# Kernel optimization log

Measured on AMD Instinct MI355X. Metric: run time of the kernel, lower is better.

Reference implementation:

```python
import jax, jax.numpy as jnp
import numpy as np

HEADS = 8
DIM_HEAD = 32
SCALE = DIM_HEAD ** -0.5


def setup_inputs() -> dict:
    key = jax.random.key(0)
    ks = jax.random.split(key, 5)
    b, c, H, W = 4, 256, 48, 48
    n = H * W
    hidden = HEADS * DIM_HEAD
    x = jax.random.normal(ks[0], (b, c, H, W), dtype=jnp.float32)
    pos_bias = jax.random.normal(ks[1], (HEADS, n, n), dtype=jnp.float32) * 0.02
    w_qkv = jax.random.normal(ks[2], (hidden * 3, c), dtype=jnp.float32) * (c ** -0.5)
    w_out = jax.random.normal(ks[3], (c, hidden), dtype=jnp.float32) * (hidden ** -0.5)
    b_out = jax.random.normal(ks[4], (c,), dtype=jnp.float32) * 0.01
    return {"x": x, "pos_bias": pos_bias, "w_qkv": w_qkv, "w_out": w_out, "b_out": b_out}


def reference(x, pos_bias, w_qkv, w_out, b_out):
    b, c, H, W = x.shape
    n = H * W
    xf = x.reshape(b, c, n)                                  # [b, c, n]
    qkv = jnp.einsum('oc,bcn->bon', w_qkv, xf)               # 1x1 conv, no bias
    q, k, v = jnp.split(qkv, 3, axis=1)                      # each [b, hidden, n]
    def to_heads(t):
        return t.reshape(b, HEADS, DIM_HEAD, n)              # b h d n
    q, k, v = to_heads(q) * SCALE, to_heads(k), to_heads(v)
    sim = jnp.einsum('bhdi,bhdj->bhij', q, k)                # [b, h, n, n]
    sim = sim + pos_bias[None]                               # broadcast over batch
    attn = jax.nn.softmax(sim, axis=-1)
    out = jnp.einsum('bhij,bhdj->bhid', attn, v)             # [b, h, n, d]
    out = out.transpose(0, 1, 3, 2).reshape(b, HEADS * DIM_HEAD, n)  # b (h d) n
    out = jnp.einsum('oc,bcn->bon', w_out, out) + b_out[None, :, None]
    return out.reshape(b, c, H, W)
```

## Files before the change

### kernel.cpp

```cpp
#include <hip/hip_runtime.h>
#include <stdint.h>
#include <stddef.h>

#define BB 4
#define CC 256
#define NH 8
#define DH 32
#define NN 2304
#define O3 768
#define HID 256
#define QK_SCALE 0.17677669529663687f
#define LOG2E 1.44269504f

typedef __attribute__((ext_vector_type(8))) short short8;
typedef __attribute__((ext_vector_type(4))) float float4v;

__device__ __forceinline__ unsigned short f2bf(float f) {
    union { float f; uint32_t u; } v; v.f = f;
    uint32_t u = v.u;
    return (unsigned short)((u + 0x7FFFu + ((u >> 16) & 1u)) >> 16);
}
__device__ __forceinline__ float bf2f(unsigned short s) {
    union { uint32_t u; float f; } v; v.u = ((uint32_t)s) << 16;
    return v.f;
}

__global__ void cast_weights(const float* __restrict__ wqkv,
                             const float* __restrict__ wout,
                             unsigned short* __restrict__ whi,
                             unsigned short* __restrict__ wlo,
                             unsigned short* __restrict__ wob) {
    int i = blockIdx.x * 256 + threadIdx.x;
    float wv = wqkv[i];
    unsigned short hi = f2bf(wv);
    whi[i] = hi;
    wlo[i] = f2bf(wv - bf2f(hi));
    if (i < HID * HID) wob[i] = f2bf(wout[i]);
}

__global__ __launch_bounds__(256) void transpose_x(const float* __restrict__ x,
                                                   unsigned short* __restrict__ xT) {
    const int n0 = blockIdx.x * 32, c0 = blockIdx.y * 32, b = blockIdx.z;
    __shared__ float ls[32][33];
    const int t = threadIdx.x;
    {
        int c = t >> 3, nc = (t & 7) * 4;
        float4 v4 = *(const float4*)(x + ((size_t)b * CC + c0 + c) * NN + n0 + nc);
        ls[c][nc] = v4.x; ls[c][nc + 1] = v4.y; ls[c][nc + 2] = v4.z; ls[c][nc + 3] = v4.w;
    }
    __syncthreads();
    {
        int n = t >> 3, cl = (t & 7) * 4;
        uint32_t p0 = (uint32_t)f2bf(ls[cl + 0][n]) | ((uint32_t)f2bf(ls[cl + 1][n]) << 16);
        uint32_t p1 = (uint32_t)f2bf(ls[cl + 2][n]) | ((uint32_t)f2bf(ls[cl + 3][n]) << 16);
        uint32_t* dst = (uint32_t*)(xT + ((size_t)b * NN + n0 + n) * CC + c0 + cl);
        dst[0] = p0; dst[1] = p1;
    }
}

__global__ __launch_bounds__(256) void qkv_gemm_bf16(const unsigned short* __restrict__ xT,
                                                     const unsigned short* __restrict__ whi,
                                                     const unsigned short* __restrict__ wlo,
                                                     unsigned short* __restrict__ q,
                                                     unsigned short* __restrict__ k,
                                                     unsigned short* __restrict__ v) {
    const int og = blockIdx.x;
    const int n0 = blockIdx.y * 64;
    const int b  = blockIdx.z;
    const int t = threadIdx.x;
    const int w = t >> 6, lane = t & 63, l15 = lane & 15, quad = lane >> 4;
    const unsigned short* xb = xT + (size_t)b * NN * CC;

    float4v acc[4] = {{0.f,0.f,0.f,0.f},{0.f,0.f,0.f,0.f},
                      {0.f,0.f,0.f,0.f},{0.f,0.f,0.f,0.f}};

    if (og < 8) {
        const int o0 = og * 64;
        const unsigned short* ap = xb + (size_t)(n0 + w * 16 + l15) * CC + quad * 8;
        #pragma unroll
        for (int c0 = 0; c0 < CC; c0 += 32) {
            short8 af = *(const short8*)(ap + c0);
            #pragma unroll
            for (int jj = 0; jj < 4; ++jj) {
                const size_t wo = (size_t)(o0 + jj * 16 + l15) * CC + c0 + quad * 8;
                short8 bh = *(const short8*)(whi + wo);
                short8 bl = *(const short8*)(wlo + wo);
                acc[jj] = __builtin_amdgcn_mfma_f32_16x16x32_bf16(af, bh, acc[jj], 0, 0, 0);
                acc[jj] = __builtin_amdgcn_mfma_f32_16x16x32_bf16(af, bl, acc[jj], 0, 0, 0);
            }
        }
        #pragma unroll
        for (int jj = 0; jj < 4; ++jj) {
            const int o = o0 + jj * 16 + l15;
            const int which = o >> 8;
            const int h = (o >> 5) & 7, d = o & 31;
            unsigned short* dst = which ? k : q;
            const float sc = which ? 1.0f : QK_SCALE * LOG2E;
            #pragma unroll
            for (int r = 0; r < 4; ++r) {
                const int n = n0 + w * 16 + quad * 4 + r;
                dst[(((size_t)b * NH + h) * NN + n) * DH + d] = f2bf(acc[jj][r] * sc);
            }
        }
    } else {
        const int o0 = 512 + (og - 8) * 64;
        const size_t wr = (size_t)(o0 + w * 16 + l15) * CC + quad * 8;
        #pragma unroll
        for (int c0 = 0; c0 < CC; c0 += 32) {
            short8 ah = *(const short8*)(whi + wr + c0);
            short8 al = *(const short8*)(wlo + wr + c0);
            #pragma unroll
            for (int jj = 0; jj < 4; ++jj) {
                short8 bf = *(const short8*)(xb + (size_t)(n0 + jj * 16 + l15) * CC + c0 + quad * 8);
                acc[jj] = __builtin_amdgcn_mfma_f32_16x16x32_bf16(ah, bf, acc[jj], 0, 0, 0);
                acc[jj] = __builtin_amdgcn_mfma_f32_16x16x32_bf16(al, bf, acc[jj], 0, 0, 0);
            }
        }
        #pragma unroll
        for (int r = 0; r < 4; ++r) {
            const int o = o0 + w * 16 + quad * 4 + r;
            const int h = (o >> 5) & 7, d = o & 31;
            #pragma unroll
            for (int jj = 0; jj < 4; ++jj) {
                const int n = n0 + jj * 16 + l15;
                v[(((size_t)b * NH + h) * DH + d) * NN + n] = f2bf(acc[jj][r]);
            }
        }
    }
}

__global__ __launch_bounds__(256) void attn_kernel(const unsigned short* __restrict__ qg,
                                                   const unsigned short* __restrict__ kg,
                                                   const unsigned short* __restrict__ vg,
                                                   const float* __restrict__ bias,
                                                   unsigned short* __restrict__ ao) {
    const int i0   = blockIdx.x * 16;
    const int h    = blockIdx.y;
    const int t    = threadIdx.x;
    const int w    = t >> 6;
    const int lane = t & 63;
    const int l15  = lane & 15;
    const int quad = lane >> 4;

    __shared__ unsigned short ps[4][16][136];

    const size_t bh = (size_t)w * NH + h;
    const unsigned short* qp = qg + bh * NN * DH;
    const unsigned short* kp = kg + bh * NN * DH;
    const unsigned short* vp = vg + bh * DH * NN;

    short8 qf = *(const short8*)(qp + (size_t)(i0 + l15) * DH + quad * 8);

    float4v oa0 = {0.f, 0.f, 0.f, 0.f};
    float4v oa1 = {0.f, 0.f, 0.f, 0.f};
    float4v zero = {0.f, 0.f, 0.f, 0.f};
    float l_r[4] = {0.f, 0.f, 0.f, 0.f};

    const float* bp = bias + ((size_t)h * NN + i0 + quad * 4) * NN + l15;

    float bcur[4][8];
    #pragma unroll
    for (int r = 0; r < 4; ++r)
        #pragma unroll
        for (int jj = 0; jj < 8; ++jj)
            bcur[r][jj] = bp[(size_t)r * NN + jj * 16] * LOG2E;

    for (int jt = 0; jt < NN; jt += 128) {
        float bnext[4][8];
        if (jt + 128 < NN) {
            #pragma unroll
            for (int r = 0; r < 4; ++r)
                #pragma unroll
                for (int jj = 0; jj < 8; ++jj)
                    bnext[r][jj] = bp[(size_t)r * NN + jt + 128 + jj * 16] * LOG2E;
        }

        float4v s[8];
        #pragma unroll
        for (int jj = 0; jj < 8; ++jj) {
            short8 kf = *(const short8*)(kp + (size_t)(jt + jj * 16 + l15) * DH + quad * 8);
            s[jj] = __builtin_amdgcn_mfma_f32_16x16x32_bf16(qf, kf, zero, 0, 0, 0);
        }

        #pragma unroll
        for (int r = 0; r < 4; ++r) {
            const int row = quad * 4 + r;
            #pragma unroll
            for (int jj = 0; jj < 8; ++jj) {
                float p = exp2f(s[jj][r] + bcur[r][jj]);
                l_r[r] += p;
                ps[w][row][jj * 16 + l15] = f2bf(p);
            }
        }

        #pragma unroll
        for (int c = 0; c < 4; ++c) {
            short8 pa = *(const short8*)&ps[w][l15][c * 32 + quad * 8];
            short8 v0 = *(const short8*)(vp + (size_t)l15 * NN        + jt + c * 32 + quad * 8);
            short8 v1 = *(const short8*)(vp + (size_t)(l15 + 16) * NN + jt + c * 32 + quad * 8);
            oa0 = __builtin_amdgcn_mfma_f32_16x16x32_bf16(pa, v0, oa0, 0, 0, 0);
            oa1 = __builtin_amdgcn_mfma_f32_16x16x32_bf16(pa, v1, oa1, 0, 0, 0);
        }

        if (jt + 128 < NN) {
            #pragma unroll
            for (int r = 0; r < 4; ++r)
                #pragma unroll
                for (int jj = 0; jj < 8; ++jj)
                    bcur[r][jj] = bnext[r][jj];
        }
    }

    #pragma unroll
    for (int r = 0; r < 4; ++r) {
        #pragma unroll
        for (int off = 1; off < 16; off <<= 1)
            l_r[r] += __shfl_xor(l_r[r], off, 64);
    }

    unsigned short* aop = ao + ((size_t)w * NN + i0) * HID + h * DH;
    #pragma unroll
    for (int r = 0; r < 4; ++r) {
        const int row = quad * 4 + r;
        const float inv = 1.0f / l_r[r];
        aop[(size_t)row * HID + l15]      = f2bf(oa0[r] * inv);
        aop[(size_t)row * HID + 16 + l15] = f2bf(oa1[r] * inv);
    }
}

__global__ __launch_bounds__(256) void out_proj(const unsigned short* __restrict__ wob,
                                                const unsigned short* __restrict__ aob,
                                                const float* __restrict__ bout,
                                                float* __restrict__ out) {
    const int n0 = blockIdx.x * 64;
    const int o0 = blockIdx.y * 64;
    const int b  = blockIdx.z;
    const int t = threadIdx.x;
    const int w = t >> 6, lane = t & 63, l15 = lane & 15, quad = lane >> 4;
    const int orow = o0 + w * 16;

    float4v acc[4] = {{0.f,0.f,0.f,0.f},{0.f,0.f,0.f,0.f},
                      {0.f,0.f,0.f,0.f},{0.f,0.f,0.f,0.f}};
    const unsigned short* ap = aob + ((size_t)b * NN + n0) * HID;
    #pragma unroll
    for (int c0 = 0; c0 < HID; c0 += 32) {
        short8 af = *(const short8*)(wob + (size_t)(orow + l15) * HID + c0 + quad * 8);
        #pragma unroll
        for (int jj = 0; jj < 4; ++jj) {
            short8 bf = *(const short8*)(ap + (size_t)(jj * 16 + l15) * HID + c0 + quad * 8);
            acc[jj] = __builtin_amdgcn_mfma_f32_16x16x32_bf16(af, bf, acc[jj], 0, 0, 0);
        }
    }
    float* op = out + (size_t)b * HID * NN;
    #pragma unroll
    for (int r = 0; r < 4; ++r) {
        const int o = orow + quad * 4 + r;
        const float bv = bout[o];
        #pragma unroll
        for (int jj = 0; jj < 4; ++jj)
            op[(size_t)o * NN + n0 + jj * 16 + l15] = acc[jj][r] + bv;
    }
}

extern "C" void kernel_launch(void* const* d_in, const int* in_sizes, int n_in,
                              void* d_out, int out_size, void* d_ws, size_t ws_size,
                              hipStream_t stream) {
    const float* x        = (const float*)d_in[0];
    const float* pos_bias = (const float*)d_in[1];
    const float* w_qkv    = (const float*)d_in[2];
    const float* w_out    = (const float*)d_in[3];
    const float* b_out    = (const float*)d_in[4];
    float* out = (float*)d_out;

    char* ws = (char*)d_ws;
    unsigned short* xT  = (unsigned short*)(ws);
    unsigned short* q   = (unsigned short*)(ws + 4718592);
    unsigned short* k   = (unsigned short*)(ws + 9437184);
    unsigned short* v   = (unsigned short*)(ws + 14155776);
    unsigned short* ao  = (unsigned short*)(ws + 18874368);
    unsigned short* wob = (unsigned short*)(ws + 23592960);
    unsigned short* whi = (unsigned short*)(ws + 23724032);
    unsigned short* wlo = (unsigned short*)(ws + 24117248);

    cast_weights<<<O3 * CC / 256, 256, 0, stream>>>(w_qkv, w_out, whi, wlo, wob);
    transpose_x<<<dim3(NN / 32, CC / 32, BB), 256, 0, stream>>>(x, xT);
    qkv_gemm_bf16<<<dim3(12, NN / 64, BB), 256, 0, stream>>>(xT, whi, wlo, q, k, v);
    attn_kernel<<<dim3(NN / 16, NH), 256, 0, stream>>>(q, k, v, pos_bias, ao);
    out_proj<<<dim3(NN / 64, HID / 64, BB), 256, 0, stream>>>(wob, ao, b_out, out);
}
```

Measured before the change: 506.5 us.

## Split attention blocks per batch, drop bias prefetch, fuse prep kernels

The attention kernel previously used 256-thread blocks where each wave handled one batch and all four waves shared the same positional-bias rows through cache. It now launches one 64-thread block per (query tile, head, batch), drops the software double-buffered bias prefetch in favour of loading bias at each tile, and merges the weight cast and x transpose into one prep kernel. This lowers register pressure and adds more independent blocks, but loses the intra-block sharing of bias loads across batches and the explicit load/compute overlap, so bias traffic may rise.

```diff
diff --git a/kernel.cpp b/kernel.cpp
--- a/kernel.cpp
+++ b/kernel.cpp
@@ -25,36 +25,38 @@
     return v.f;
 }
 
-__global__ void cast_weights(const float* __restrict__ wqkv,
-                             const float* __restrict__ wout,
-                             unsigned short* __restrict__ whi,
-                             unsigned short* __restrict__ wlo,
-                             unsigned short* __restrict__ wob) {
-    int i = blockIdx.x * 256 + threadIdx.x;
-    float wv = wqkv[i];
-    unsigned short hi = f2bf(wv);
-    whi[i] = hi;
-    wlo[i] = f2bf(wv - bf2f(hi));
-    if (i < HID * HID) wob[i] = f2bf(wout[i]);
-}
-
-__global__ __launch_bounds__(256) void transpose_x(const float* __restrict__ x,
-                                                   unsigned short* __restrict__ xT) {
-    const int n0 = blockIdx.x * 32, c0 = blockIdx.y * 32, b = blockIdx.z;
-    __shared__ float ls[32][33];
+__global__ __launch_bounds__(256) void prep_kernel(const float* __restrict__ x,
+                                                   const float* __restrict__ wqkv,
+                                                   const float* __restrict__ wout,
+                                                   unsigned short* __restrict__ xT,
+                                                   unsigned short* __restrict__ whi,
+                                                   unsigned short* __restrict__ wlo,
+                                                   unsigned short* __restrict__ wob) {
+    const int bid = blockIdx.x;
     const int t = threadIdx.x;
-    {
-        int c = t >> 3, nc = (t & 7) * 4;
-        float4 v4 = *(const float4*)(x + ((size_t)b * CC + c0 + c) * NN + n0 + nc);
-        ls[c][nc] = v4.x; ls[c][nc + 1] = v4.y; ls[c][nc + 2] = v4.z; ls[c][nc + 3] = v4.w;
-    }
-    __syncthreads();
-    {
-        int n = t >> 3, cl = (t & 7) * 4;
-        uint32_t p0 = (uint32_t)f2bf(ls[cl + 0][n]) | ((uint32_t)f2bf(ls[cl + 1][n]) << 16);
-        uint32_t p1 = (uint32_t)f2bf(ls[cl + 2][n]) | ((uint32_t)f2bf(ls[cl + 3][n]) << 16);
-        uint32_t* dst = (uint32_t*)(xT + ((size_t)b * NN + n0 + n) * CC + c0 + cl);
-        dst[0] = p0; dst[1] = p1;
+    if (bid < 2304) {
+        const int n0 = (bid % 72) * 32, c0 = ((bid / 72) % 8) * 32, b = bid / 576;
+        __shared__ float ls[32][33];
+        {
+            int c = t >> 3, nc = (t & 7) * 4;
+            float4 v4 = *(const float4*)(x + ((size_t)b * CC + c0 + c) * NN + n0 + nc);
+            ls[c][nc] = v4.x; ls[c][nc + 1] = v4.y; ls[c][nc + 2] = v4.z; ls[c][nc + 3] = v4.w;
+        }
+        __syncthreads();
+        {
+            int n = t >> 3, cl = (t & 7) * 4;
+            uint32_t p0 = (uint32_t)f2bf(ls[cl + 0][n]) | ((uint32_t)f2bf(ls[cl + 1][n]) << 16);
+            uint32_t p1 = (uint32_t)f2bf(ls[cl + 2][n]) | ((uint32_t)f2bf(ls[cl + 3][n]) << 16);
+            uint32_t* dst = (uint32_t*)(xT + ((size_t)b * NN + n0 + n) * CC + c0 + cl);
+            dst[0] = p0; dst[1] = p1;
+        }
+    } else {
+        int i = (bid - 2304) * 256 + t;
+        float wv = wqkv[i];
+        unsigned short hi = f2bf(wv);
+        whi[i] = hi;
+        wlo[i] = f2bf(wv - bf2f(hi));
+        if (i < HID * HID) wob[i] = f2bf(wout[i]);
     }
 }
 
@@ -129,22 +131,21 @@
     }
 }
 
-__global__ __launch_bounds__(256) void attn_kernel(const unsigned short* __restrict__ qg,
-                                                   const unsigned short* __restrict__ kg,
-                                                   const unsigned short* __restrict__ vg,
-                                                   const float* __restrict__ bias,
-                                                   unsigned short* __restrict__ ao) {
+__global__ __launch_bounds__(64) void attn_kernel(const unsigned short* __restrict__ qg,
+                                                  const unsigned short* __restrict__ kg,
+                                                  const unsigned short* __restrict__ vg,
+                                                  const float* __restrict__ bias,
+                                                  unsigned short* __restrict__ ao) {
     const int i0   = blockIdx.x * 16;
     const int h    = blockIdx.y;
-    const int t    = threadIdx.x;
-    const int w    = t >> 6;
-    const int lane = t & 63;
+    const int b    = blockIdx.z;
+    const int lane = threadIdx.x;
     const int l15  = lane & 15;
     const int quad = lane >> 4;
 
-    __shared__ unsigned short ps[4][16][136];
-
-    const size_t bh = (size_t)w * NH + h;
+    __shared__ unsigned short ps[16][136];
+
+    const size_t bh = (size_t)b * NH + h;
     const unsigned short* qp = qg + bh * NN * DH;
     const unsigned short* kp = kg + bh * NN * DH;
     const unsigned short* vp = vg + bh * DH * NN;
@@ -158,22 +159,13 @@
 
     const float* bp = bias + ((size_t)h * NN + i0 + quad * 4) * NN + l15;
 
-    float bcur[4][8];
-    #pragma unroll
-    for (int r = 0; r < 4; ++r)
-        #pragma unroll
-        for (int jj = 0; jj < 8; ++jj)
-            bcur[r][jj] = bp[(size_t)r * NN + jj * 16] * LOG2E;
-
     for (int jt = 0; jt < NN; jt += 128) {
-        float bnext[4][8];
-        if (jt + 128 < NN) {
-            #pragma unroll
-            for (int r = 0; r < 4; ++r)
-                #pragma unroll
-                for (int jj = 0; jj < 8; ++jj)
-                    bnext[r][jj] = bp[(size_t)r * NN + jt + 128 + jj * 16] * LOG2E;
-        }
+        float bcur[4][8];
+        #pragma unroll
+        for (int r = 0; r < 4; ++r)
+            #pragma unroll
+            for (int jj = 0; jj < 8; ++jj)
+                bcur[r][jj] = bp[(size_t)r * NN + jt + jj * 16] * LOG2E;
 
         float4v s[8];
         #pragma unroll
@@ -189,26 +181,18 @@
             for (int jj = 0; jj < 8; ++jj) {
                 float p = exp2f(s[jj][r] + bcur[r][jj]);
                 l_r[r] += p;
-                ps[w][row][jj * 16 + l15] = f2bf(p);
+                ps[row][jj * 16 + l15] = f2bf(p);
             }
         }
 
         #pragma unroll
         for (int c = 0; c < 4; ++c) {
-            short8 pa = *(const short8*)&ps[w][l15][c * 32 + quad * 8];
+            short8 pa = *(const short8*)&ps[l15][c * 32 + quad * 8];
             short8 v0 = *(const short8*)(vp + (size_t)l15 * NN        + jt + c * 32 + quad * 8);
             short8 v1 = *(const short8*)(vp + (size_t)(l15 + 16) * NN + jt + c * 32 + quad * 8);
             oa0 = __builtin_amdgcn_mfma_f32_16x16x32_bf16(pa, v0, oa0, 0, 0, 0);
             oa1 = __builtin_amdgcn_mfma_f32_16x16x32_bf16(pa, v1, oa1, 0, 0, 0);
         }
-
-        if (jt + 128 < NN) {
-            #pragma unroll
-            for (int r = 0; r < 4; ++r)
-                #pragma unroll
-                for (int jj = 0; jj < 8; ++jj)
-                    bcur[r][jj] = bnext[r][jj];
-        }
     }
 
     #pragma unroll
@@ -218,7 +202,7 @@
             l_r[r] += __shfl_xor(l_r[r], off, 64);
     }
 
-    unsigned short* aop = ao + ((size_t)w * NN + i0) * HID + h * DH;
+    unsigned short* aop = ao + ((size_t)b * NN + i0) * HID + h * DH;
     #pragma unroll
     for (int r = 0; r < 4; ++r) {
         const int row = quad * 4 + r;
@@ -273,18 +257,17 @@
     float* out = (float*)d_out;
 
     char* ws = (char*)d_ws;
-    unsigned short* xT  = (unsigned short*)(ws);
-    unsigned short* q   = (unsigned short*)(ws + 4718592);
-    unsigned short* k   = (unsigned short*)(ws + 9437184);
-    unsigned short* v   = (unsigned short*)(ws + 14155776);
-    unsigned short* ao  = (unsigned short*)(ws + 18874368);
-    unsigned short* wob = (unsigned short*)(ws + 23592960);
-    unsigned short* whi = (unsigned short*)(ws + 23724032);
-    unsigned short* wlo = (unsigned short*)(ws + 24117248);
-
-    cast_weights<<<O3 * CC / 256, 256, 0, stream>>>(w_qkv, w_out, whi, wlo, wob);
-    transpose_x<<<dim3(NN / 32, CC / 32, BB), 256, 0, stream>>>(x, xT);
+    unsigned short* q   = (unsigned short*)(ws);
+    unsigned short* k   = (unsigned short*)(ws + 4718592);
+    unsigned short* v   = (unsigned short*)(ws + 9437184);
+    unsigned short* ao  = (unsigned short*)(ws + 14155776);
+    unsigned short* wob = (unsigned short*)(ws + 18874368);
+    unsigned short* whi = (unsigned short*)(ws + 19005440);
+    unsigned short* wlo = (unsigned short*)(ws + 19398656);
+    unsigned short* xT  = (unsigned short*)(ws + 19791872);
+
+    prep_kernel<<<3072, 256, 0, stream>>>(x, w_qkv, w_out, xT, whi, wlo, wob);
     qkv_gemm_bf16<<<dim3(12, NN / 64, BB), 256, 0, stream>>>(xT, whi, wlo, q, k, v);
-    attn_kernel<<<dim3(NN / 16, NH), 256, 0, stream>>>(q, k, v, pos_bias, ao);
+    attn_kernel<<<dim3(NN / 16, NH, BB), 64, 0, stream>>>(q, k, v, pos_bias, ao);
     out_proj<<<dim3(NN / 64, HID / 64, BB), 256, 0, stream>>>(wob, ao, b_out, out);
 }
```

Measured after the change: 462.3 us. -8.7%, faster.
